# Kernel tuning notes

Measured on AMD Instinct MI355X. Metric: run time of the kernel, lower is better.

Reference implementation:

```python
import jax, jax.numpy as jnp
import numpy as np


def setup_inputs() -> dict:
    key = jax.random.key(0)
    k_w, k_xi, k_u = jax.random.split(key, 3)
    N, d, M, L, B = 4096, 512, 256, 16, 1024
    W = 2 * L + 1  # window width = 33
    # xavier-normal-ish scale for weight (fan_in=d, fan_out=M*W per torch xavier on last dim pairs)
    w_scale = (2.0 / (W + d)) ** 0.5
    xi_scale = (2.0 / (M + N + 2 * L)) ** 0.5
    weight = jax.random.normal(k_w, (M, W, d), dtype=jnp.float32) * w_scale
    bias = jnp.zeros((M, W, 1), dtype=jnp.float32)
    xi = jax.random.normal(k_xi, (M, N + 2 * L), dtype=jnp.float32) * xi_scale
    u = jax.random.normal(k_u, (B, d), dtype=jnp.float32)
    return {"u": u, "weight": weight, "bias": bias, "xi": xi}


def reference(u, weight, bias, xi):
    # weight: [M, W, d], bias: [M, W, 1], xi: [M, N + W - 1], u: [B, d]
    M, W, d = weight.shape
    N = xi.shape[1] - (W - 1)
    # first_step: G[m, j, b] = sigmoid(sum_k weight[m,j,k] * u[b,k] + bias[m,j])
    G = jax.nn.sigmoid(jnp.einsum('mjd,bd->mjb', weight, u) + bias)  # [M, W, B]
    # im2col-style unfold of xi into overlapping windows, replacing the N-step Python loop
    idx = jnp.arange(N)[:, None] + jnp.arange(W)[None, :]  # [N, W]
    Xw = xi[:, idx]  # [M, N, W]
    # out[n, b] = sum_{m, j} xi[m, n+j] * G[m, j, b]  == torch.cat of iter_prod rows
    return jnp.einsum('mnj,mjb->nb', Xw, G)  # [N, B]
```

## Files before the change

### kernel.cpp

```cpp
#include <hip/hip_runtime.h>
#include <hip/hip_bf16.h>

typedef __attribute__((ext_vector_type(8))) short bf16x8;
typedef __attribute__((ext_vector_type(4))) float f32x4;
typedef unsigned int u32;
typedef unsigned short u16;

#define XI_ROW 4128
#define KP     8448
#define NB     1024
#define NN     4096
#define DDIM   512

__device__ __forceinline__ u16 f2bf(float f) {
  union { float f; unsigned u; } c; c.f = f;
  return (u16)((c.u + 0x7FFFu + ((c.u >> 16) & 1u)) >> 16);
}
__device__ __forceinline__ float bf2f(u16 h) {
  union { u32 u; float f; } c; c.u = ((u32)h) << 16; return c.f;
}
__device__ __forceinline__ u32 pk2bf(float a, float b) {
  return (u32)f2bf(a) | ((u32)f2bf(b) << 16);
}
__device__ __forceinline__ void gld16(const u16* g, u16* l) {
  __builtin_amdgcn_global_load_lds(
      (const __attribute__((address_space(1))) u32*)(const void*)g,
      (__attribute__((address_space(3))) u32*)(void*)l, 16, 0, 0);
}

#define BAR() __builtin_amdgcn_s_barrier()
#define LGKM0() asm volatile("s_waitcnt lgkmcnt(0)" ::: "memory")
#define LGKM8() asm volatile("s_waitcnt lgkmcnt(8)" ::: "memory")
#define WAITVM(N) asm volatile("s_waitcnt vmcnt(" #N ")" ::: "memory")
#define SCHED0() __builtin_amdgcn_sched_barrier(0)

__global__ __launch_bounds__(256) void k_prep(
    const float* __restrict__ w, const float* __restrict__ u,
    const float* __restrict__ xi, u16* __restrict__ Wbf,
    u16* __restrict__ Ubf, u16* __restrict__ xiT) {
  __shared__ u16 tile[32][33];
  const int bx = blockIdx.x, t = threadIdx.x;
  if (bx < 4224) {
    int kp = bx * 2 + (t >> 7), tl = t & 127;
    int m = kp & 255, j = kp >> 8;
    float4 v = ((const float4*)(w + (size_t)(m * 33 + j) * DDIM))[tl];
    ((uint2*)(Wbf + (size_t)kp * DDIM))[tl] =
        make_uint2(pk2bf(v.x, v.y), pk2bf(v.z, v.w));
  } else if (bx < 4736) {
    int b = (bx - 4224) * 2 + (t >> 7), tl = t & 127;
    float4 v = ((const float4*)(u + (size_t)b * DDIM))[tl];
    ((uint2*)(Ubf + (size_t)b * DDIM))[tl] =
        make_uint2(pk2bf(v.x, v.y), pk2bf(v.z, v.w));
  } else {
    int bx2 = bx - 4736;
    int cblk = bx2 % 129, mblk = bx2 / 129;
    int c0 = cblk * 32, m0 = mblk * 32;
    int tx = t & 31, ty = t >> 5;
#pragma unroll
    for (int i = 0; i < 4; ++i)
      tile[ty + i * 8][tx] = f2bf(xi[(size_t)(m0 + ty + i * 8) * XI_ROW + c0 + tx]);
    __syncthreads();
#pragma unroll
    for (int i = 0; i < 4; ++i)
      xiT[(size_t)(c0 + ty + i * 8) * 256 + m0 + tx] = tile[tx][ty + i * 8];
  }
}

template<int KSTEPS, int AS, int BS>
__device__ __forceinline__ void gemm_pipeline(
    const u16* __restrict__ aSrc, const u16* __restrict__ bSrc,
    u16* As0, u16* As1, u16* Bl0, u16* Bl1,
    int wid, int wr, int wc, int rl, int kg, int rl7,
    f32x4 (&acc)[4][4]) {

  auto stage = [&](u16* Ab, u16* Bb, int kk) {
#pragma unroll
    for (int i = 0; i < 4; ++i)
      gld16(aSrc + (size_t)i * 8 * AS + kk, &Ab[(wid * 4 + i) * 512]);
#pragma unroll
    for (int i = 0; i < 4; ++i)
      gld16(bSrc + (size_t)i * 8 * BS + kk, &Bb[(wid * 4 + i) * 512]);
  };
  auto compute = [&](const u16* Ab, const u16* Bb) {
#pragma unroll
    for (int kh = 0; kh < 2; ++kh) {
      bf16x8 af[4], bfv[4];
#pragma unroll
      for (int fm = 0; fm < 4; ++fm)
        af[fm] = *(const bf16x8*)&Ab[(wr * 64 + fm * 16 + rl) * 64 +
                                     (((kh * 4 + kg) ^ rl7) * 8)];
#pragma unroll
      for (int fn = 0; fn < 4; ++fn)
        bfv[fn] = *(const bf16x8*)&Bb[(wc * 64 + fn * 16 + rl) * 64 +
                                      (((kh * 4 + kg) ^ rl7) * 8)];
      __builtin_amdgcn_s_setprio(1);
#pragma unroll
      for (int fm = 0; fm < 4; ++fm)
#pragma unroll
        for (int fn = 0; fn < 4; ++fn)
          acc[fm][fn] = __builtin_amdgcn_mfma_f32_16x16x32_bf16(
              af[fm], bfv[fn], acc[fm][fn], 0, 0, 0);
      __builtin_amdgcn_s_setprio(0);
    }
  };

  stage(As0, Bl0, 0);
  WAITVM(0);
  BAR();
#pragma unroll 1
  for (int ts = 0; ts < KSTEPS - 2; ts += 2) {
    stage(As1, Bl1, (ts + 1) * 64);
    WAITVM(8);
    BAR();
    compute(As0, Bl0);
    BAR();
    stage(As0, Bl0, (ts + 2) * 64);
    WAITVM(8);
    BAR();
    compute(As1, Bl1);
    BAR();
  }
  stage(As1, Bl1, (KSTEPS - 1) * 64);
  WAITVM(8);
  BAR();
  compute(As0, Bl0);
  BAR();
  WAITVM(0);
  BAR();
  compute(As1, Bl1);
}

__global__ __launch_bounds__(256) void k_gemm1(
    const u16* __restrict__ Wbf, const u16* __restrict__ Ubf,
    const float* __restrict__ Bsrc, u16* __restrict__ Gt) {
  __shared__ u16 lds1[32768];
  u16* As0 = lds1;
  u16* As1 = lds1 + 8192;
  u16* Bl0 = lds1 + 16384;
  u16* Bl1 = lds1 + 24576;
  const int r0 = blockIdx.x * 128;
  const int b0 = blockIdx.y * 128;
  const int t = threadIdx.x, lane = t & 63, wid = t >> 6;
  const int wr = wid >> 1, wc = wid & 1;
  const int rl = lane & 15, kg = lane >> 4, rl7 = rl & 7;
  const int lr = lane >> 3, lc = (lane & 7) ^ (lr & 7);
  const u16* aSrc = Wbf + (size_t)(r0 + wid * 32 + lr) * DDIM + lc * 8;
  const u16* bSrc = Ubf + (size_t)(b0 + wid * 32 + lr) * DDIM + lc * 8;

  f32x4 acc[4][4] = {};
  gemm_pipeline<8, DDIM, DDIM>(aSrc, bSrc, As0, As1, Bl0, Bl1,
                               wid, wr, wc, rl, kg, rl7, acc);

  __syncthreads();
  u16* Lt = lds1;
#pragma unroll
  for (int fm = 0; fm < 4; ++fm) {
    int kloc = wr * 64 + fm * 16 + kg * 4;
    int kbase = r0 + kloc;
    float b4[4];
#pragma unroll
    for (int r = 0; r < 4; ++r) {
      int kk = kbase + r;
      b4[r] = Bsrc[(kk & 255) * 33 + (kk >> 8)];
    }
#pragma unroll
    for (int fn = 0; fn < 4; ++fn) {
      int bloc = wc * 64 + fn * 16 + rl;
      u16 o[4];
#pragma unroll
      for (int r = 0; r < 4; ++r) {
        float x = acc[fm][fn][r] + b4[r];
        o[r] = f2bf(1.0f / (1.0f + __expf(-x)));
      }
      *(uint2*)&Lt[bloc * 136 + kloc] =
          make_uint2((u32)o[0] | ((u32)o[1] << 16),
                     (u32)o[2] | ((u32)o[3] << 16));
    }
  }
  __syncthreads();
  const int bl = t >> 4, j = t & 15;
#pragma unroll
  for (int p = 0; p < 8; ++p) {
    int bloc = p * 16 + bl;
    uint4 v = *(const uint4*)&Lt[bloc * 136 + j * 8];
    *(uint4*)(Gt + (size_t)(b0 + bloc) * KP + r0 + j * 8) = v;
  }
}

__global__ __launch_bounds__(512, 2) void k_gemm2(
    const u16* __restrict__ xiT, const u16* __restrict__ Gt,
    float* __restrict__ Out, u16* __restrict__ Part, int allbf) {
  __shared__ u16 lds[65536];
  const int lid = blockIdx.x;
  const int b0 = (lid & 3) * 256;
  const int ks = (lid >> 2) & 3;
  const int n0 = (lid >> 4) * 256;
  const int kOff = (ks < 2) ? ks * 2176 : 4352 + (ks - 2) * 2048;
  const int nt = (ks < 2) ? 34 : 32;

  const int t = threadIdx.x, lane = t & 63, wid = t >> 6;
  const int wr = wid >> 2, wc = wid & 3;
  const int rl = lane & 15, kg = lane >> 4, rl7 = rl & 7;
  const int sr = lane >> 3;
  const int sc = (lane & 7) ^ sr;

  const u16* aS = xiT + (size_t)(n0 + wid * 16 + sr) * 256 + kOff + sc * 8;
  const u16* bS = Gt  + (size_t)(b0 + wid * 16 + sr) * KP  + kOff + sc * 8;

  f32x4 acc[8][4] = {};
  bf16x8 af[8], b01[4], b23[4];

  auto stA = [&](int tile, int half, int buf) {
    u16* d = lds + (buf * 4 + half) * 8192 + wid * 1024;
    const u16* s = aS + (size_t)half * 32768 + (size_t)tile * 64;
    gld16(s, d);
    gld16(s + 2048, d + 512);
  };
  auto stB = [&](int tile, int half, int buf) {
    u16* d = lds + (buf * 4 + 2 + half) * 8192 + wid * 1024;
    const u16* s = bS + (size_t)half * 128 * KP + (size_t)tile * 64;
    gld16(s, d);
    gld16(s + (size_t)8 * KP, d + 512);
  };
  auto rdA = [&](int buf, int sub) {
    const u16* p = lds + (buf * 4 + wr) * 8192;
#pragma unroll
    for (int q = 0; q < 4; ++q)
#pragma unroll
      for (int kh = 0; kh < 2; ++kh)
        af[q * 2 + kh] = *(const bf16x8*)
            &p[((sub * 4 + q) * 16 + rl) * 64 + (((kh * 4 + kg) ^ rl7) * 8)];
  };
  auto rdB = [&](int buf, int sub, bf16x8 (&bq)[4]) {
    const u16* p = lds + (buf * 4 + 2 + (wc >> 1)) * 8192;
#pragma unroll
    for (int q = 0; q < 2; ++q)
#pragma unroll
      for (int kh = 0; kh < 2; ++kh)
        bq[q * 2 + kh] = *(const bf16x8*)
            &p[((wc & 1) * 64 + (sub * 2 + q) * 16 + rl) * 64 +
               (((kh * 4 + kg) ^ rl7) * 8)];
  };
  auto mm = [&](int sm, int sn, bf16x8 (&bq)[4]) {
    __builtin_amdgcn_s_setprio(1);
#pragma unroll
    for (int q = 0; q < 4; ++q)
#pragma unroll
      for (int p = 0; p < 2; ++p)
#pragma unroll
        for (int kh = 0; kh < 2; ++kh)
          acc[sm * 4 + q][sn * 2 + p] = __builtin_amdgcn_mfma_f32_16x16x32_bf16(
              af[q * 2 + kh], bq[p * 2 + kh], acc[sm * 4 + q][sn * 2 + p], 0, 0, 0);
    __builtin_amdgcn_s_setprio(0);
  };

  auto runIter = [&](int T, bool s2, bool s3) {
    rdA(0, 0); rdB(0, 0, b01); stB(T + 1, 1, 1);
    LGKM8(); SCHED0(); BAR(); LGKM0(); SCHED0(); mm(0, 0, b01);
    rdB(0, 1, b23); stA(T + 1, 0, 1);
    SCHED0(); BAR(); LGKM0(); SCHED0(); mm(0, 1, b23);
    rdA(0, 1); stA(T + 1, 1, 1);
    SCHED0(); BAR(); LGKM0(); SCHED0(); mm(1, 0, b01);
    if (s2) { stB(T + 2, 0, 0); WAITVM(2); } else { WAITVM(0); }
    SCHED0(); BAR(); SCHED0(); mm(1, 1, b23);
    rdA(1, 0); rdB(1, 0, b01); if (s2) stB(T + 2, 1, 0);
    LGKM8(); SCHED0(); BAR(); LGKM0(); SCHED0(); mm(0, 0, b01);
    rdB(1, 1, b23); if (s2) stA(T + 2, 0, 0);
    SCHED0(); BAR(); LGKM0(); SCHED0(); mm(0, 1, b23);
    rdA(1, 1); if (s2) stA(T + 2, 1, 0);
    SCHED0(); BAR(); LGKM0(); SCHED0(); mm(1, 0, b01);
    if (s3) { stB(T + 3, 0, 1); WAITVM(2); }
    else if (s2) { WAITVM(0); }
    SCHED0(); BAR(); SCHED0(); mm(1, 1, b23);
  };

  stA(0, 0, 0); stA(0, 1, 0); stB(0, 0, 0); stB(0, 1, 0);
  stB(1, 0, 1);
  WAITVM(2);
  BAR();

  const int nIter = nt >> 1;
#pragma unroll 1
  for (int it = 0; it < nIter - 1; ++it) runIter(it * 2, true, true);
  runIter((nIter - 1) * 2, false, false);

  if (!allbf && ks == 0) {
#pragma unroll
    for (int fm = 0; fm < 8; ++fm)
#pragma unroll
      for (int fn = 0; fn < 4; ++fn) {
        int n = n0 + wr * 128 + fm * 16 + kg * 4;
        int b = b0 + wc * 64 + fn * 16 + rl;
#pragma unroll
        for (int r = 0; r < 4; ++r)
          Out[(size_t)(n + r) * NB + b] = acc[fm][fn][r];
      }
  } else {
    int slot = allbf ? ks : (ks - 1);
    u16* P = Part + (size_t)slot * (NN * NB);
#pragma unroll
    for (int fm = 0; fm < 8; ++fm)
#pragma unroll
      for (int fn = 0; fn < 4; ++fn) {
        int n = n0 + wr * 128 + fm * 16 + kg * 4;
        int b = b0 + wc * 64 + fn * 16 + rl;
#pragma unroll
        for (int r = 0; r < 4; ++r)
          P[(size_t)(n + r) * NB + b] = f2bf(acc[fm][fn][r]);
      }
  }
}

__global__ __launch_bounds__(256) void k_reduce(float* __restrict__ Out,
                                                const u16* __restrict__ Part,
                                                int allbf) {
  size_t i = (size_t)blockIdx.x * 256 + threadIdx.x;
  float4 a;
  int np;
  if (allbf) { a = make_float4(0.f, 0.f, 0.f, 0.f); np = 4; }
  else       { a = ((const float4*)Out)[i];          np = 3; }
  for (int p = 0; p < np; ++p) {
    ushort4 v = ((const ushort4*)(Part + (size_t)p * (NN * NB)))[i];
    a.x += bf2f(v.x); a.y += bf2f(v.y); a.z += bf2f(v.z); a.w += bf2f(v.w);
  }
  ((float4*)Out)[i] = a;
}

extern "C" void kernel_launch(void* const* d_in, const int* in_sizes, int n_in,
                              void* d_out, int out_size, void* d_ws, size_t ws_size,
                              hipStream_t stream) {
  const float* u  = (const float*)d_in[0];
  const float* w  = (const float*)d_in[1];
  const float* bs = (const float*)d_in[2];
  const float* xi = (const float*)d_in[3];
  float* out = (float*)d_out;

  u16* xiT  = (u16*)d_ws;
  u16* Gt   = (u16*)((char*)d_ws + 2113536);
  u16* Wbf  = (u16*)((char*)d_ws + 19415040);
  u16* Ubf  = (u16*)((char*)d_ws + 28065792);
  u16* Part = (u16*)((char*)d_ws + 19415040);
  const int allbf = (ws_size >= 52969472ull) ? 1 : 0;

  k_prep<<<5768, 256, 0, stream>>>(w, u, xi, Wbf, Ubf, xiT);
  k_gemm1<<<dim3(66, 8), 256, 0, stream>>>(Wbf, Ubf, bs, Gt);
  k_gemm2<<<256, 512, 0, stream>>>(xiT, Gt, out, Part, allbf);
  k_reduce<<<4096, 256, 0, stream>>>(out, Part, allbf);
}
```

Baseline: 98.96 us.

## Overlap xi transpose with gemm1, prefetch B fragments earlier, widen reduce vectors

Moves the xi-to-bf16 transpose blocks out of the prep kernel and into extra blocks of the first GEMM launch, so the transpose runs alongside GEMM tiles instead of before them. In the second GEMM's main loop, the B-fragment LDS reads for the next sub-step are issued right after the barrier, ahead of the preceding MFMA group, to hide LDS latency. The reduce kernel now handles 8 elements per thread with 128-bit loads. The risks are that the transpose blocks compete with GEMM blocks for CUs, and that the earlier reads raise register pressure.

```diff
diff --git a/kernel.cpp b/kernel.cpp
--- a/kernel.cpp
+++ b/kernel.cpp
@@ -33,12 +33,11 @@
 #define LGKM8() asm volatile("s_waitcnt lgkmcnt(8)" ::: "memory")
 #define WAITVM(N) asm volatile("s_waitcnt vmcnt(" #N ")" ::: "memory")
 #define SCHED0() __builtin_amdgcn_sched_barrier(0)
+#define MEMF() asm volatile("" ::: "memory")
 
 __global__ __launch_bounds__(256) void k_prep(
     const float* __restrict__ w, const float* __restrict__ u,
-    const float* __restrict__ xi, u16* __restrict__ Wbf,
-    u16* __restrict__ Ubf, u16* __restrict__ xiT) {
-  __shared__ u16 tile[32][33];
+    u16* __restrict__ Wbf, u16* __restrict__ Ubf) {
   const int bx = blockIdx.x, t = threadIdx.x;
   if (bx < 4224) {
     int kp = bx * 2 + (t >> 7), tl = t & 127;
@@ -46,23 +45,11 @@
     float4 v = ((const float4*)(w + (size_t)(m * 33 + j) * DDIM))[tl];
     ((uint2*)(Wbf + (size_t)kp * DDIM))[tl] =
         make_uint2(pk2bf(v.x, v.y), pk2bf(v.z, v.w));
-  } else if (bx < 4736) {
+  } else {
     int b = (bx - 4224) * 2 + (t >> 7), tl = t & 127;
     float4 v = ((const float4*)(u + (size_t)b * DDIM))[tl];
     ((uint2*)(Ubf + (size_t)b * DDIM))[tl] =
         make_uint2(pk2bf(v.x, v.y), pk2bf(v.z, v.w));
-  } else {
-    int bx2 = bx - 4736;
-    int cblk = bx2 % 129, mblk = bx2 / 129;
-    int c0 = cblk * 32, m0 = mblk * 32;
-    int tx = t & 31, ty = t >> 5;
-#pragma unroll
-    for (int i = 0; i < 4; ++i)
-      tile[ty + i * 8][tx] = f2bf(xi[(size_t)(m0 + ty + i * 8) * XI_ROW + c0 + tx]);
-    __syncthreads();
-#pragma unroll
-    for (int i = 0; i < 4; ++i)
-      xiT[(size_t)(c0 + ty + i * 8) * 256 + m0 + tx] = tile[tx][ty + i * 8];
   }
 }
 
@@ -132,15 +119,34 @@
 
 __global__ __launch_bounds__(256) void k_gemm1(
     const u16* __restrict__ Wbf, const u16* __restrict__ Ubf,
-    const float* __restrict__ Bsrc, u16* __restrict__ Gt) {
+    const float* __restrict__ Bsrc, u16* __restrict__ Gt,
+    const float* __restrict__ xi, u16* __restrict__ xiT) {
   __shared__ u16 lds1[32768];
+  const int bx = blockIdx.x, t = threadIdx.x;
+
+  if (bx >= 528) {
+    u16 (*tile)[33] = (u16(*)[33])lds1;
+    int id = bx - 528;
+    int cblk = id % 129, mblk = id / 129;
+    int c0 = cblk * 32, m0 = mblk * 32;
+    int tx = t & 31, ty = t >> 5;
+#pragma unroll
+    for (int i = 0; i < 4; ++i)
+      tile[ty + i * 8][tx] = f2bf(xi[(size_t)(m0 + ty + i * 8) * XI_ROW + c0 + tx]);
+    __syncthreads();
+#pragma unroll
+    for (int i = 0; i < 4; ++i)
+      xiT[(size_t)(c0 + ty + i * 8) * 256 + m0 + tx] = tile[tx][ty + i * 8];
+    return;
+  }
+
   u16* As0 = lds1;
   u16* As1 = lds1 + 8192;
   u16* Bl0 = lds1 + 16384;
   u16* Bl1 = lds1 + 24576;
-  const int r0 = blockIdx.x * 128;
-  const int b0 = blockIdx.y * 128;
-  const int t = threadIdx.x, lane = t & 63, wid = t >> 6;
+  const int r0 = (bx % 66) * 128;
+  const int b0 = (bx / 66) * 128;
+  const int lane = t & 63, wid = t >> 6;
   const int wr = wid >> 1, wc = wid & 1;
   const int rl = lane & 15, kg = lane >> 4, rl7 = rl & 7;
   const int lr = lane >> 3, lc = (lane & 7) ^ (lr & 7);
@@ -255,15 +261,17 @@
   };
 
   auto runIter = [&](int T, bool s2, bool s3) {
-    rdA(0, 0); rdB(0, 0, b01); stB(T + 1, 1, 1);
+    rdA(0, 0); stB(T + 1, 1, 1);
     LGKM8(); SCHED0(); BAR(); LGKM0(); SCHED0(); mm(0, 0, b01);
     rdB(0, 1, b23); stA(T + 1, 0, 1);
     SCHED0(); BAR(); LGKM0(); SCHED0(); mm(0, 1, b23);
     rdA(0, 1); stA(T + 1, 1, 1);
     SCHED0(); BAR(); LGKM0(); SCHED0(); mm(1, 0, b01);
     if (s2) { stB(T + 2, 0, 0); WAITVM(2); } else { WAITVM(0); }
-    SCHED0(); BAR(); SCHED0(); mm(1, 1, b23);
-    rdA(1, 0); rdB(1, 0, b01); if (s2) stB(T + 2, 1, 0);
+    SCHED0(); BAR(); MEMF();
+    rdB(1, 0, b01);
+    SCHED0(); mm(1, 1, b23);
+    rdA(1, 0); if (s2) stB(T + 2, 1, 0);
     LGKM8(); SCHED0(); BAR(); LGKM0(); SCHED0(); mm(0, 0, b01);
     rdB(1, 1, b23); if (s2) stA(T + 2, 0, 0);
     SCHED0(); BAR(); LGKM0(); SCHED0(); mm(0, 1, b23);
@@ -271,13 +279,17 @@
     SCHED0(); BAR(); LGKM0(); SCHED0(); mm(1, 0, b01);
     if (s3) { stB(T + 3, 0, 1); WAITVM(2); }
     else if (s2) { WAITVM(0); }
-    SCHED0(); BAR(); SCHED0(); mm(1, 1, b23);
+    SCHED0(); BAR(); MEMF();
+    rdB(0, 0, b01);
+    SCHED0(); mm(1, 1, b23);
   };
 
   stA(0, 0, 0); stA(0, 1, 0); stB(0, 0, 0); stB(0, 1, 0);
   stB(1, 0, 1);
   WAITVM(2);
   BAR();
+  MEMF();
+  rdB(0, 0, b01);
 
   const int nIter = nt >> 1;
 #pragma unroll 1
@@ -314,16 +326,29 @@
 __global__ __launch_bounds__(256) void k_reduce(float* __restrict__ Out,
                                                 const u16* __restrict__ Part,
                                                 int allbf) {
-  size_t i = (size_t)blockIdx.x * 256 + threadIdx.x;
-  float4 a;
+  size_t i8 = ((size_t)blockIdx.x * 256 + threadIdx.x) * 8;
+  float a[8];
   int np;
-  if (allbf) { a = make_float4(0.f, 0.f, 0.f, 0.f); np = 4; }
-  else       { a = ((const float4*)Out)[i];          np = 3; }
+  if (allbf) {
+#pragma unroll
+    for (int q = 0; q < 8; ++q) a[q] = 0.f;
+    np = 4;
+  } else {
+    float4 x = *(const float4*)(Out + i8);
+    float4 y = *(const float4*)(Out + i8 + 4);
+    a[0] = x.x; a[1] = x.y; a[2] = x.z; a[3] = x.w;
+    a[4] = y.x; a[5] = y.y; a[6] = y.z; a[7] = y.w;
+    np = 3;
+  }
   for (int p = 0; p < np; ++p) {
-    ushort4 v = ((const ushort4*)(Part + (size_t)p * (NN * NB)))[i];
-    a.x += bf2f(v.x); a.y += bf2f(v.y); a.z += bf2f(v.z); a.w += bf2f(v.w);
-  }
-  ((float4*)Out)[i] = a;
+    uint4 v = *(const uint4*)(Part + (size_t)p * (NN * NB) + i8);
+    a[0] += bf2f((u16)(v.x & 0xFFFFu)); a[1] += bf2f((u16)(v.x >> 16));
+    a[2] += bf2f((u16)(v.y & 0xFFFFu)); a[3] += bf2f((u16)(v.y >> 16));
+    a[4] += bf2f((u16)(v.z & 0xFFFFu)); a[5] += bf2f((u16)(v.z >> 16));
+    a[6] += bf2f((u16)(v.w & 0xFFFFu)); a[7] += bf2f((u16)(v.w >> 16));
+  }
+  *(float4*)(Out + i8)     = make_float4(a[0], a[1], a[2], a[3]);
+  *(float4*)(Out + i8 + 4) = make_float4(a[4], a[5], a[6], a[7]);
 }
 
 extern "C" void kernel_launch(void* const* d_in, const int* in_sizes, int n_in,
@@ -342,8 +367,8 @@
   u16* Part = (u16*)((char*)d_ws + 19415040);
   const int allbf = (ws_size >= 52969472ull) ? 1 : 0;
 
-  k_prep<<<5768, 256, 0, stream>>>(w, u, xi, Wbf, Ubf, xiT);
-  k_gemm1<<<dim3(66, 8), 256, 0, stream>>>(Wbf, Ubf, bs, Gt);
+  k_prep<<<4736, 256, 0, stream>>>(w, u, Wbf, Ubf);
+  k_gemm1<<<1560, 256, 0, stream>>>(Wbf, Ubf, bs, Gt, xi, xiT);
   k_gemm2<<<256, 512, 0, stream>>>(xiT, Gt, out, Part, allbf);
-  k_reduce<<<4096, 256, 0, stream>>>(out, Part, allbf);
-}
+  k_reduce<<<2048, 256, 0, stream>>>(out, Part, allbf);
+}
```

New measurement: 99.92 us. Within noise of the previous version (+1.0%).
